# Performance work log

Measured on AMD Instinct MI355X. Metric: run time of the kernel, lower is better.

The kernel has to match this reference:

```python
import jax, jax.numpy as jnp
import numpy as np

N_WAY = 5
K_SHOT = 5
NBNN_TOPK = 3
TEMPERATURE = 2.0
EPS = 1e-8


def setup_inputs() -> dict:
    key = jax.random.key(0)
    k1, k2, k3 = jax.random.split(key, 3)
    b, q, c, h, w = 4, 75, 640, 11, 11
    s = N_WAY * K_SHOT
    support_xf = jax.random.normal(k1, (b, s, c, h, w), jnp.float32)
    query_xf = jax.random.normal(k2, (b, q, c, h, w), jnp.float32)
    # episodes are ordered class-major: [way0 shots..., way1 shots..., ...]
    support_y = jnp.tile(jnp.repeat(jnp.arange(N_WAY, dtype=jnp.int32), K_SHOT)[None, :], (b, 1))
    query_y = jax.random.randint(k3, (b, q), 0, N_WAY, dtype=jnp.int32)
    return {"support_xf": support_xf, "query_xf": query_xf,
            "support_y": support_y, "query_y": query_y}


def _mn4_loss(support_xf, query_xf, query_y):
    b, s, c, h, w = support_xf.shape
    q = query_xf.shape[1]
    M_q = h * w
    M_s = K_SHOT * h * w

    # ---- InnerproductSimilarity (cosine) ----
    # support: [b, N, c, M_s]  (class-major grouping of shots)
    sf = support_xf.reshape(b, N_WAY, K_SHOT, c, h * w).transpose(0, 1, 3, 2, 4).reshape(b, N_WAY, c, M_s)
    qf = query_xf.reshape(b, q, c, M_q)
    sf = sf / (jnp.linalg.norm(sf, axis=2, keepdims=True) + EPS)
    qf = qf / (jnp.linalg.norm(qf, axis=2, keepdims=True) + EPS)
    # simi: [b, q, N, M_q, M_s]
    simi = jnp.einsum('bqcm,bncs->bqnms', qf, sf)

    # ---- _MNN (compensate_for_single=True branch) ----
    # merged view: [b, q, M_q, N*M_s]
    merged = simi.transpose(0, 1, 3, 2, 4).reshape(b, q, M_q, N_WAY * M_s)
    query_nearest = jnp.argmax(merged, axis=-1)          # [b, q, M_q]
    class_wise_max = simi.max(-1).max(2) + 1.0           # [b, q, M_q]
    class_m = jax.nn.one_hot(query_nearest, N_WAY * M_s, dtype=simi.dtype) * class_wise_max[..., None]
    support_nearest = jnp.argmax(class_m, axis=-2)       # [b, q, N*M_s]
    gathered = jnp.take_along_axis(support_nearest, query_nearest, axis=-1)  # [b, q, M_q]
    q_mask = (gathered == jnp.arange(M_q)[None, None, :])                    # [b, q, M_q]

    # ---- NBNN value: topk over support descriptors, masked sum over query descriptors ----
    topv = jax.lax.top_k(simi, NBNN_TOPK)[0].mean(-1)    # [b, q, N, M_q]
    query_value = (topv * q_mask[:, :, None, :].astype(topv.dtype)).sum(-1)  # [b, q, N]
    logits = query_value.reshape(b * q, N_WAY) / TEMPERATURE

    # ---- cross entropy (mean) ----
    logp = jax.nn.log_softmax(logits, axis=-1)
    y = query_y.reshape(-1)
    loss = -jnp.take_along_axis(logp, y[:, None], axis=1).mean()
    return loss


def reference(support_xf, query_xf, support_y, query_y):
    del support_y  # episodes are class-major by construction
    return _mn4_loss(support_xf, query_xf, query_y)
```

## Files before the change

### kernel.cpp

```cpp
#include <hip/hip_runtime.h>
#include <hip/hip_bf16.h>
#include <math.h>

#define BB 4
#define QQ 75
#define NBQ 300
#define CC 640
#define HW 121
#define NW 5
#define KS 5
#define SS 25
#define MS 605
#define JT 3025
#define BQ_PER_XCD 38

typedef __attribute__((ext_vector_type(8))) short short8;
typedef __attribute__((ext_vector_type(4))) float f32x4;

#define OFF_SBF   0
#define SBF_F     (BB*JT*CC/2)
#define OFF_QBF   (OFF_SBF + SBF_F)
#define QBF_F     (NBQ*HW*CC/2)
#define OFF_P     (OFF_QBF + QBF_F)

__device__ __forceinline__ void async16(const void* g, void* l) {
    __builtin_amdgcn_global_load_lds(
        (const __attribute__((address_space(1))) unsigned int*)g,
        (__attribute__((address_space(3))) unsigned int*)l, 16, 0, 0);
}

__global__ void prep_kernel(const float* __restrict__ sup, const float* __restrict__ qry,
                            __hip_bfloat16* __restrict__ Sbf, __hip_bfloat16* __restrict__ Qbf,
                            float* __restrict__ out)
{
    const int col = blockIdx.x;
    const int t   = threadIdx.x;
    if (col == 0 && t == 0) out[0] = 0.f;
    const float* src;
    __hip_bfloat16* dst;
    if (col < BB * SS) {
        const int b = col / SS, s = col % SS;
        const int n = s / KS, k = s % KS;
        src = sup + (size_t)col * (CC * HW);
        dst = Sbf + ((size_t)b * JT + n * MS + k * HW) * CC;
    } else {
        const int bq = col - BB * SS;
        src = qry + (size_t)bq * (CC * HW);
        dst = Qbf + (size_t)bq * (HW * CC);
    }

    __shared__ float inv[128];
    __shared__ float T[32][128];

    const int cc2 = t >> 7, hw1 = t & 127;
    float ss0 = 0.f, ss1 = 0.f;
    if (hw1 < HW) {
        const float* p = src + hw1;
#pragma unroll 16
        for (int c = cc2; c < CC; c += 4) {
            float v0 = p[(size_t)c * HW];
            float v1 = p[(size_t)(c + 2) * HW];
            ss0 = fmaf(v0, v0, ss0);
            ss1 = fmaf(v1, v1, ss1);
        }
    }
    T[cc2][hw1] = ss0 + ss1;
    __syncthreads();
    if (t < 128) inv[t] = (t < HW) ? 1.f / (sqrtf(T[0][t] + T[1][t]) + 1e-8f) : 0.f;

    for (int c0 = 0; c0 < CC; c0 += 32) {
        __syncthreads();
#pragma unroll
        for (int i = 0; i < 16; ++i) {
            int idx = t + i * 256;
            int cc = idx >> 7, hw = idx & 127;
            if (hw < HW) T[cc][hw] = src[(size_t)(c0 + cc) * HW + hw] * inv[hw];
        }
        __syncthreads();
        const int hw = t >> 1, half = t & 1;
        if (hw < HW) {
            __hip_bfloat16 hv[16];
#pragma unroll
            for (int i = 0; i < 16; ++i) hv[i] = __float2bfloat16(T[half * 16 + i][hw]);
            int4* op = reinterpret_cast<int4*>(dst + (size_t)hw * CC + c0 + half * 16);
            op[0] = reinterpret_cast<int4*>(hv)[0];
            op[1] = reinterpret_cast<int4*>(hv)[1];
        }
    }
}

__launch_bounds__(256, 3)
__global__ void simi_kernel(const __hip_bfloat16* __restrict__ Sbf,
                            const __hip_bfloat16* __restrict__ Qbf,
                            float4* __restrict__ pout)
{
    const int xcd   = blockIdx.x & 7;
    const int local = blockIdx.x >> 3;
    const int n     = local % NW;
    const int bq    = xcd * BQ_PER_XCD + local / NW;
    if (bq >= NBQ) return;
    const int b   = bq / QQ;
    const int tid = threadIdx.x;
    const int lane = tid & 63, wid = tid >> 6;
    const int l15 = lane & 15, l4 = lane >> 4;
    const int wj0 = (wid & 1) * 64;
    const int wm0 = (wid >> 1) * 64;

    const unsigned short* qbase = (const unsigned short*)(Qbf + (size_t)bq * (HW * CC));
    const unsigned short* sbase = (const unsigned short*)(Sbf + ((size_t)b * JT + n * MS) * CC);

    __shared__ __align__(16) unsigned short AsBuf[2][128 * 32];
    __shared__ __align__(16) unsigned short BsBuf[2][128 * 32];

    const int srow = lane >> 2;
    const int kb   = (lane & 3) ^ ((lane >> 3) & 3);
    int aoff2[2];
#pragma unroll
    for (int g = 0; g < 2; ++g) {
        int arow = wid * 32 + g * 16 + srow;
        int grow = arow < HW ? arow : HW - 1;
        aoff2[g] = grow * CC + kb * 8;
    }
    int jb2[2];
#pragma unroll
    for (int g = 0; g < 2; ++g) jb2[g] = wid * 32 + g * 16 + srow;

    const int ldso_base = wid * 2048 + lane * 16;

#define STAGE(ms0_, c0_, nb_)                                                        \
    {                                                                                \
        _Pragma("unroll")                                                            \
        for (int g = 0; g < 2; ++g) {                                                \
            const int ldso = ldso_base + g * 1024;                                   \
            async16(qbase + aoff2[g] + (c0_), (char*)&AsBuf[nb_][0] + ldso);         \
            int j_ = (ms0_) + jb2[g];                                                \
            int jc_ = j_ < MS ? j_ : MS - 1;                                         \
            async16(sbase + jc_ * CC + kb * 8 + (c0_), (char*)&BsBuf[nb_][0] + ldso);\
        }                                                                            \
    }

    float rt0[4], rt1[4], rt2[4]; int ra[4];
#pragma unroll
    for (int i = 0; i < 4; ++i) { rt0[i] = -INFINITY; rt1[i] = -INFINITY; rt2[i] = -INFINITY; ra[i] = 0; }

    f32x4 acc[4][4];
#pragma unroll
    for (int ji = 0; ji < 4; ++ji)
#pragma unroll
        for (int qi = 0; qi < 4; ++qi)
#pragma unroll
            for (int r = 0; r < 4; ++r) acc[ji][qi][r] = 0.f;

    STAGE(0, 0, 0);
    int nb = 0;

    const int slot = l4 ^ ((l15 >> 1) & 3);
    const int aro  = (wm0 + l15) * 32 + slot * 8;
    const int bro  = (wj0 + l15) * 32 + slot * 8;

    for (int t = 0; t < 100; ++t) {
        const int tn = t + 1;
        if (tn < 100) {
            const int nms = (tn / 20) * 128;
            const int nc  = (tn % 20) * 32;
            STAGE(nms, nc, nb ^ 1);
            asm volatile("s_waitcnt vmcnt(4)" ::: "memory");
        } else {
            asm volatile("s_waitcnt vmcnt(0)" ::: "memory");
        }
        __builtin_amdgcn_s_barrier();

        short8 af[4], bf[4];
#pragma unroll
        for (int qi = 0; qi < 4; ++qi)
            af[qi] = *(const short8*)(&AsBuf[nb][0] + aro + qi * 512);
#pragma unroll
        for (int ji = 0; ji < 4; ++ji)
            bf[ji] = *(const short8*)(&BsBuf[nb][0] + bro + ji * 512);

        __builtin_amdgcn_s_setprio(1);
#pragma unroll
        for (int ji = 0; ji < 4; ++ji)
#pragma unroll
            for (int qi = 0; qi < 4; ++qi)
                acc[ji][qi] = __builtin_amdgcn_mfma_f32_16x16x32_bf16(
                    bf[ji], af[qi], acc[ji][qi], 0, 0, 0);
        __builtin_amdgcn_s_setprio(0);
        nb ^= 1;

        if ((t % 20) == 19) {
            const int ms0 = (t / 20) * 128;
#pragma unroll
            for (int qi = 0; qi < 4; ++qi)
#pragma unroll
                for (int ji = 0; ji < 4; ++ji)
#pragma unroll
                    for (int r = 0; r < 4; ++r) {
                        const int jl = ms0 + wj0 + ji * 16 + l4 * 4 + r;
                        float v = (jl < MS) ? acc[ji][qi][r] : -INFINITY;
                        const bool gt = v > rt0[qi];
                        ra[qi] = gt ? (n * MS + jl) : ra[qi];
                        const float m1 = fminf(rt0[qi], v);
                        rt0[qi] = fmaxf(rt0[qi], v);
                        const float m2 = fminf(rt1[qi], m1);
                        rt1[qi] = fmaxf(rt1[qi], m1);
                        rt2[qi] = fmaxf(rt2[qi], m2);
                    }
#pragma unroll
            for (int ji = 0; ji < 4; ++ji)
#pragma unroll
                for (int qi = 0; qi < 4; ++qi)
#pragma unroll
                    for (int r = 0; r < 4; ++r) acc[ji][qi][r] = 0.f;
        }

        __builtin_amdgcn_s_barrier();
    }

#pragma unroll
    for (int qi = 0; qi < 4; ++qi) {
#pragma unroll
        for (int mask = 16; mask <= 32; mask <<= 1) {
            const float o0 = __shfl_xor(rt0[qi], mask);
            const float o1 = __shfl_xor(rt1[qi], mask);
            const float o2 = __shfl_xor(rt2[qi], mask);
            const int   oa = __shfl_xor(ra[qi],  mask);
            const bool take = (o0 > rt0[qi]) || (o0 == rt0[qi] && oa < ra[qi]);
            ra[qi] = take ? oa : ra[qi];
            float m1 = fminf(rt0[qi], o0); rt0[qi] = fmaxf(rt0[qi], o0);
            float m2 = fminf(rt1[qi], m1); rt1[qi] = fmaxf(rt1[qi], m1);
            rt2[qi] = fmaxf(rt2[qi], m2);
            m1 = fminf(rt0[qi], o1); rt0[qi] = fmaxf(rt0[qi], o1);
            m2 = fminf(rt1[qi], m1); rt1[qi] = fmaxf(rt1[qi], m1);
            rt2[qi] = fmaxf(rt2[qi], m2);
            m1 = fminf(rt0[qi], o2); rt0[qi] = fmaxf(rt0[qi], o2);
            m2 = fminf(rt1[qi], m1); rt1[qi] = fmaxf(rt1[qi], m1);
            rt2[qi] = fmaxf(rt2[qi], m2);
        }
    }

    __syncthreads();
    float4* mbuf = (float4*)&AsBuf[0][0];
    if ((wid & 1) == 0 && l4 == 0) {
#pragma unroll
        for (int qi = 0; qi < 4; ++qi) {
            float4 v; v.x = rt0[qi]; v.y = rt1[qi]; v.z = rt2[qi];
            v.w = __int_as_float(ra[qi]);
            mbuf[wm0 + qi * 16 + l15] = v;
        }
    }
    __syncthreads();
    if ((wid & 1) == 1 && l4 == 0) {
#pragma unroll
        for (int qi = 0; qi < 4; ++qi) {
            const int m = wm0 + qi * 16 + l15;
            const float4 o = mbuf[m];
            const int oa = __float_as_int(o.w);
            float s0 = rt0[qi], s1 = rt1[qi], s2 = rt2[qi]; int sa = ra[qi];
            const bool take = (o.x > s0) || (o.x == s0 && oa < sa);
            sa = take ? oa : sa;
            float m1 = fminf(s0, o.x); s0 = fmaxf(s0, o.x);
            float m2 = fminf(s1, m1);  s1 = fmaxf(s1, m1);
            s2 = fmaxf(s2, m2);
            m1 = fminf(s0, o.y); s0 = fmaxf(s0, o.y);
            m2 = fminf(s1, m1);  s1 = fmaxf(s1, m1);
            s2 = fmaxf(s2, m2);
            m1 = fminf(s0, o.z); s0 = fmaxf(s0, o.z);
            m2 = fminf(s1, m1);  s1 = fmaxf(s1, m1);
            s2 = fmaxf(s2, m2);
            if (m < HW) {
                float4 v; v.x = s0; v.y = s1; v.z = s2; v.w = __int_as_float(sa);
                pout[(bq * NW + n) * HW + m] = v;
            }
        }
    }
#undef STAGE
}

__global__ void merge_kernel(const float4* __restrict__ pout, const int* __restrict__ qy,
                             float* __restrict__ out)
{
    const int bq  = blockIdx.x;
    const int tid = threadIdx.x;

    __shared__ float cw[128];
    __shared__ int   ag[128];
    __shared__ float tv[NW][128];
    __shared__ float maskf[128];
    __shared__ float lg[8];

    if (tid < HW) {
        float g0 = -INFINITY; int garg = 0;
#pragma unroll
        for (int n = 0; n < NW; ++n) {
            const float4 a = pout[(bq * NW + n) * HW + tid];
            if (a.x > g0) { g0 = a.x; garg = __float_as_int(a.w); }
            tv[n][tid] = (a.x + a.y + a.z) * (1.f / 3.f);
        }
        cw[tid] = g0 + 1.0f;
        ag[tid] = garg;
    }
    __syncthreads();
    if (tid < HW) {
        const float mycw = cw[tid];
        const int   myag = ag[tid];
        float ok = 1.f;
        for (int m2 = 0; m2 < HW; ++m2) {
            if (m2 == tid) continue;
            if (ag[m2] == myag) {
                float c2 = cw[m2];
                if (c2 > mycw || (c2 == mycw && m2 < tid)) ok = 0.f;
            }
        }
        maskf[tid] = ok;
    }
    __syncthreads();
    if (tid < NW) {
        float s = 0.f;
        for (int mq = 0; mq < HW; ++mq) s += maskf[mq] * tv[tid][mq];
        lg[tid] = s * 0.5f;
    }
    __syncthreads();
    if (tid == 0) {
        float m = lg[0];
#pragma unroll
        for (int n2 = 1; n2 < NW; ++n2) m = fmaxf(m, lg[n2]);
        float se = 0.f;
#pragma unroll
        for (int n2 = 0; n2 < NW; ++n2) se += expf(lg[n2] - m);
        int y = qy[bq];
        atomicAdd(out, -(lg[y] - m - logf(se)) * (1.f / NBQ));
    }
}

extern "C" void kernel_launch(void* const* d_in, const int* in_sizes, int n_in,
                              void* d_out, int out_size, void* d_ws, size_t ws_size,
                              hipStream_t stream)
{
    const float* sup = (const float*)d_in[0];
    const float* qry = (const float*)d_in[1];
    const int*   qy  = (const int*)d_in[3];
    float* out = (float*)d_out;
    float* ws  = (float*)d_ws;

    __hip_bfloat16* Sbf = (__hip_bfloat16*)(ws + OFF_SBF);
    __hip_bfloat16* Qbf = (__hip_bfloat16*)(ws + OFF_QBF);
    float4* pout = (float4*)(ws + OFF_P);

    hipLaunchKernelGGL(prep_kernel, dim3(BB * SS + NBQ), dim3(256), 0, stream,
                       sup, qry, Sbf, Qbf, out);
    hipLaunchKernelGGL(simi_kernel, dim3(8 * BQ_PER_XCD * NW), dim3(256), 0, stream,
                       Sbf, Qbf, pout);
    hipLaunchKernelGGL(merge_kernel, dim3(NBQ), dim3(128), 0, stream, pout, qy, out);
}
```

Before: 395.0 us.

## Split prep into separate norm and scale kernels with 4x more blocks

The fused prep kernel, which computed per-column norms and then scaled and converted to bf16, is split in two. A norm kernel writes partial sums of squares per channel quarter, and a scale kernel has each block convert one quarter of the channels. This raises block count from 400 to 1600 per kernel to fill more CUs. The cost is an extra launch and reading the fp32 inputs twice from memory. The norm scratch reuses the pout region, which is safe because simi writes pout only later.

```diff
diff --git a/kernel.cpp b/kernel.cpp
--- a/kernel.cpp
+++ b/kernel.cpp
@@ -22,6 +22,7 @@
 #define OFF_QBF   (OFF_SBF + SBF_F)
 #define QBF_F     (NBQ*HW*CC/2)
 #define OFF_P     (OFF_QBF + QBF_F)
+#define OFF_NRM   OFF_P
 
 __device__ __forceinline__ void async16(const void* g, void* l) {
     __builtin_amdgcn_global_load_lds(
@@ -29,13 +30,35 @@
         (__attribute__((address_space(3))) unsigned int*)l, 16, 0, 0);
 }
 
-__global__ void prep_kernel(const float* __restrict__ sup, const float* __restrict__ qry,
-                            __hip_bfloat16* __restrict__ Sbf, __hip_bfloat16* __restrict__ Qbf,
-                            float* __restrict__ out)
-{
-    const int col = blockIdx.x;
+__global__ void norm_kernel(const float* __restrict__ sup, const float* __restrict__ qry,
+                            float* __restrict__ nrm, float* __restrict__ out)
+{
+    const int blk = blockIdx.x;
+    const int col = blk >> 2, r = blk & 3;
+    const int hw  = threadIdx.x;
+    if (blk == 0 && hw == 0) out[0] = 0.f;
+    const float* src = (col < BB * SS)
+        ? sup + (size_t)col * (CC * HW)
+        : qry + (size_t)(col - BB * SS) * (CC * HW);
+    float ss = 0.f;
+    if (hw < HW) {
+        const float* p = src + hw;
+#pragma unroll 16
+        for (int i = 0; i < CC / 4; ++i) {
+            const float v = p[(size_t)(r + i * 4) * HW];
+            ss = fmaf(v, v, ss);
+        }
+    }
+    nrm[((size_t)col * 4 + r) * 128 + hw] = ss;
+}
+
+__global__ void scale_kernel(const float* __restrict__ sup, const float* __restrict__ qry,
+                             const float* __restrict__ nrm,
+                             __hip_bfloat16* __restrict__ Sbf, __hip_bfloat16* __restrict__ Qbf)
+{
+    const int blk = blockIdx.x;
+    const int col = blk >> 2, qtr = blk & 3;
     const int t   = threadIdx.x;
-    if (col == 0 && t == 0) out[0] = 0.f;
     const float* src;
     __hip_bfloat16* dst;
     if (col < BB * SS) {
@@ -52,23 +75,16 @@
     __shared__ float inv[128];
     __shared__ float T[32][128];
 
-    const int cc2 = t >> 7, hw1 = t & 127;
-    float ss0 = 0.f, ss1 = 0.f;
-    if (hw1 < HW) {
-        const float* p = src + hw1;
-#pragma unroll 16
-        for (int c = cc2; c < CC; c += 4) {
-            float v0 = p[(size_t)c * HW];
-            float v1 = p[(size_t)(c + 2) * HW];
-            ss0 = fmaf(v0, v0, ss0);
-            ss1 = fmaf(v1, v1, ss1);
-        }
-    }
-    T[cc2][hw1] = ss0 + ss1;
-    __syncthreads();
-    if (t < 128) inv[t] = (t < HW) ? 1.f / (sqrtf(T[0][t] + T[1][t]) + 1e-8f) : 0.f;
-
-    for (int c0 = 0; c0 < CC; c0 += 32) {
+    if (t < 128) {
+        const float p0 = nrm[((size_t)col * 4 + 0) * 128 + t];
+        const float p1 = nrm[((size_t)col * 4 + 1) * 128 + t];
+        const float p2 = nrm[((size_t)col * 4 + 2) * 128 + t];
+        const float p3 = nrm[((size_t)col * 4 + 3) * 128 + t];
+        inv[t] = (t < HW) ? 1.f / (sqrtf((p0 + p2) + (p1 + p3)) + 1e-8f) : 0.f;
+    }
+
+    for (int it = 0; it < 5; ++it) {
+        const int c0 = qtr * 160 + it * 32;
         __syncthreads();
 #pragma unroll
         for (int i = 0; i < 16; ++i) {
@@ -346,9 +362,12 @@
     __hip_bfloat16* Sbf = (__hip_bfloat16*)(ws + OFF_SBF);
     __hip_bfloat16* Qbf = (__hip_bfloat16*)(ws + OFF_QBF);
     float4* pout = (float4*)(ws + OFF_P);
-
-    hipLaunchKernelGGL(prep_kernel, dim3(BB * SS + NBQ), dim3(256), 0, stream,
-                       sup, qry, Sbf, Qbf, out);
+    float*  nrm  = (float*)(ws + OFF_NRM);
+
+    hipLaunchKernelGGL(norm_kernel,  dim3((BB * SS + NBQ) * 4), dim3(128), 0, stream,
+                       sup, qry, nrm, out);
+    hipLaunchKernelGGL(scale_kernel, dim3((BB * SS + NBQ) * 4), dim3(256), 0, stream,
+                       sup, qry, nrm, Sbf, Qbf);
     hipLaunchKernelGGL(simi_kernel, dim3(8 * BQ_PER_XCD * NW), dim3(256), 0, stream,
                        Sbf, Qbf, pout);
     hipLaunchKernelGGL(merge_kernel, dim3(NBQ), dim3(128), 0, stream, pout, qy, out);
```

New measurement: 406.8 us. 1.03x slower.
